# Optimization experiments

Measured on AMD Instinct MI355X. Metric: run time of the kernel, lower is better.

## Reference

```python
import jax, jax.numpy as jnp
import numpy as np

DIM = 512
HID = 2048
E = 16
B = 8
N = 2048
THRESHOLD = 0.8
CAP_FACTOR = 2.0  # eval mode
MIN_EXPERT_CAPACITY = 4
LOSS_COEF = 0.01
CAP = max(MIN_EXPERT_CAPACITY, min(N, int(N * CAP_FACTOR / E)))  # 256


def setup_inputs() -> dict:
    key = jax.random.key(0)
    k1, k2, k3, k4 = jax.random.split(key, 4)
    x = jax.random.normal(k1, (B, N, DIM), dtype=jnp.float32)
    w_gating = jax.random.normal(k2, (DIM, E), dtype=jnp.float32)
    std1 = 1.0 / np.sqrt(HID)
    std2 = 1.0 / np.sqrt(DIM)
    w1 = jax.random.uniform(k3, (E, DIM, HID), jnp.float32, -std1, std1)
    w2 = jax.random.uniform(k4, (E, HID, DIM), jnp.float32, -std2, std2)
    return {"x": x, "w_gating": w_gating, "w1": w1, "w2": w2}


def _gate(x, w_gating):
    # raw gate probabilities [B, N, E]
    raw = jax.nn.softmax(jnp.einsum('bnd,de->bne', x, w_gating), axis=-1)
    order = jnp.argsort(-raw, axis=-1)                      # descending sort indices
    sp = jnp.take_along_axis(raw, order, axis=-1)           # sorted probs (desc)
    cum = jnp.cumsum(sp, axis=-1)
    tm = cum >= THRESHOLD
    k = jnp.argmax(tm.astype(jnp.float32), axis=-1) + 1     # dynamic k per token
    k = jnp.where(jnp.any(tm, axis=-1), k, E)
    # select top-k in sorted order, renormalize
    rank = jnp.arange(E)
    sel = (rank < k[..., None]).astype(raw.dtype)           # [B,N,E] sorted order
    selp = sp * sel
    normp = selp / jnp.sum(selp, axis=-1, keepdims=True)
    # scatter back to expert order via inverse permutation
    inv = jnp.argsort(order, axis=-1)
    mask = jnp.take_along_axis(sel, inv, axis=-1)           # expert_masks [B,N,E]
    weights = jnp.take_along_axis(normp, inv, axis=-1)      # expert_weights
    # capacity: exclusive cumsum over tokens
    pos = (jnp.cumsum(mask, axis=-2) - mask) * mask
    mask = mask * (pos < float(CAP)).astype(mask.dtype)
    pos = pos * mask
    pos_tok = jnp.sum(pos, axis=-1).astype(jnp.int32)       # [B,N] (summed across experts, as in source)
    in_cap = (pos_tok < CAP).astype(raw.dtype)
    oh = jax.nn.one_hot(pos_tok, CAP, dtype=raw.dtype) * in_cap[..., None]  # [B,N,CAP]
    dispatch = mask[..., None] * oh[..., None, :]           # [B,N,E,CAP]
    combine = (weights * mask)[..., None] * oh[..., None, :]
    density = jnp.mean(mask, axis=-2)
    density_proxy = jnp.mean(raw, axis=-2)
    loss = jnp.mean(density_proxy * density) * float(E * E)
    loss = loss + 0.0 * jnp.mean(k.astype(jnp.float32))
    return dispatch, combine, loss


def reference(x, w_gating, w1, w2):
    dispatch, combine, loss = _gate(x, w_gating)
    expert_inputs = jnp.einsum('bnd,bnec->ebcd', x, dispatch)        # [E,B,CAP,D]
    ei = expert_inputs.reshape(E, B * CAP, DIM)
    hidden = jax.nn.gelu(jnp.einsum('end,edh->enh', ei, w1), approximate=False)
    eo = jnp.einsum('enh,ehd->end', hidden, w2).reshape(E, B, CAP, DIM)
    output = jnp.einsum('ebcd,bnec->bnd', eo, combine)               # [B,N,D]
    return output, loss * LOSS_COEF
```

## Files before the change

kernel.cpp:

```cpp
#include <hip/hip_runtime.h>
#include <math.h>

#define DIMC 512
#define HIDC 2048
#define EC   16
#define BC   8
#define NC   2048
#define CAPC 256
#define BN   (BC * NC)
#define THRESH 0.8f

typedef unsigned short u16;
typedef __attribute__((ext_vector_type(8))) __bf16 bf16x8;
typedef __attribute__((ext_vector_type(4))) float f32x4;

__device__ __forceinline__ float bf2f(unsigned u) {
    union { unsigned i; float f; } v; v.i = u << 16; return v.f;
}
__device__ __forceinline__ u16 f2bf(float f) {
    union { float f; unsigned i; } v; v.f = f;
    unsigned r = v.i + 0x7fff + ((v.i >> 16) & 1);
    return (u16)(r >> 16);
}
__device__ __forceinline__ float gelu_f(float x) {
    float u = 0.7978845608028654f * (x + 0.044715f * x * x * x);
    float t = __expf(2.f * u);
    float th = 1.f - 2.f / (t + 1.f);
    return 0.5f * x * (1.f + th);
}

__global__ void init_kernel(int* __restrict__ heads, int* __restrict__ pos_tok)
{
    int i = blockIdx.x * 256 + threadIdx.x;
    if (i < EC * BC * CAPC) heads[i] = -1;
    if (i < BN) pos_tok[i] = 0;
}

__global__ __launch_bounds__(256) void gate_kernel(const float* __restrict__ x,
                                                   const float* __restrict__ wg,
                                                   float* __restrict__ raw,
                                                   float* __restrict__ weights,
                                                   float* __restrict__ maskf)
{
    __shared__ float wlds[16][516];
    __shared__ float lg[16][16];
    int t = threadIdx.x;
    int tok16 = t >> 4, e = t & 15;
    int token = blockIdx.x * 16 + tok16;

    {
        const float4* wg4 = (const float4*)wg;
#pragma unroll
        for (int j = 0; j < 8; ++j) {
            int idx4 = j * 256 + t;
            float4 v = wg4[idx4];
            int d  = idx4 >> 2;
            int e0 = (idx4 & 3) * 4;
            wlds[e0 + 0][d] = v.x;
            wlds[e0 + 1][d] = v.y;
            wlds[e0 + 2][d] = v.z;
            wlds[e0 + 3][d] = v.w;
        }
    }
    __syncthreads();

    const float4* xr = (const float4*)(x + (size_t)token * DIMC);
    const float4* wl = (const float4*)&wlds[e][0];
    float a0 = 0.f, a1 = 0.f, a2 = 0.f, a3 = 0.f;
#pragma unroll 4
    for (int i = 0; i < 128; i += 4) {
        float4 xa = xr[i], xb = xr[i+1], xc = xr[i+2], xd = xr[i+3];
        float4 wa = wl[i], wb = wl[i+1], wc = wl[i+2], wd = wl[i+3];
        a0 = fmaf(xa.w, wa.w, fmaf(xa.z, wa.z, fmaf(xa.y, wa.y, fmaf(xa.x, wa.x, a0))));
        a1 = fmaf(xb.w, wb.w, fmaf(xb.z, wb.z, fmaf(xb.y, wb.y, fmaf(xb.x, wb.x, a1))));
        a2 = fmaf(xc.w, wc.w, fmaf(xc.z, wc.z, fmaf(xc.y, wc.y, fmaf(xc.x, wc.x, a2))));
        a3 = fmaf(xd.w, wd.w, fmaf(xd.z, wd.z, fmaf(xd.y, wd.y, fmaf(xd.x, wd.x, a3))));
    }
    float logit = (a0 + a1) + (a2 + a3);

    float m = logit;
#pragma unroll
    for (int off = 8; off >= 1; off >>= 1) m = fmaxf(m, __shfl_xor(m, off, 16));
    float p = expf(logit - m);
    float s = p;
#pragma unroll
    for (int off = 8; off >= 1; off >>= 1) s += __shfl_xor(s, off, 16);
    p = p / s;

    int rank = 0;
    float cum = p;
#pragma unroll
    for (int j = 1; j < 16; ++j) {
        float op = __shfl_xor(p, j, 16);
        int oidx = e ^ j;
        bool ahead = (op > p) || (op == p && oidx < e);
        if (ahead) { rank++; cum += op; }
    }
    bool tm = (cum >= THRESH);
    int kr = tm ? rank : (EC - 1);
#pragma unroll
    for (int off = 8; off >= 1; off >>= 1) kr = min(kr, __shfl_xor(kr, off, 16));
    bool sel = (rank <= kr);

    float dsel = sel ? p : 0.f;
    float denom = dsel;
#pragma unroll
    for (int off = 8; off >= 1; off >>= 1) denom += __shfl_xor(denom, off, 16);
    float w = sel ? (p / denom) : 0.f;

    size_t o = (size_t)token * EC + e;
    raw[o]     = p;
    weights[o] = w;
    maskf[o]   = sel ? 1.f : 0.f;
    (void)lg;
}

__global__ __launch_bounds__(64) void capacity_kernel(const float* __restrict__ raw,
                                                      float* __restrict__ maskf,
                                                      int* __restrict__ pos,
                                                      int* __restrict__ pos_tok,
                                                      float* __restrict__ density,
                                                      float* __restrict__ proxy)
{
    int t = blockIdx.x;
    int b = t / EC, e = t % EC;
    int lane = threadIdx.x;

    size_t idx = ((size_t)b * NC + lane) * EC + e;
    const size_t step = (size_t)64 * EC;
    float mv = maskf[idx];
    float rv = raw[idx];

    int count = 0;
    float rsum = 0.f;
    for (int n0 = 0; n0 < NC; n0 += 64) {
        float mn = 0.f, rn = 0.f;
        if (n0 + 64 < NC) { mn = maskf[idx + step]; rn = raw[idx + step]; }

        rsum += rv;
        unsigned long long bal = __ballot(mv != 0.f);
        int below = __popcll(bal & ((1ull << lane) - 1ull));
        int pval = 0;
        if (mv != 0.f) {
            pval = count + below;
            if (pval >= CAPC) { maskf[idx] = 0.f; pval = 0; }
            else if (pval > 0) atomicAdd(&pos_tok[b * NC + n0 + lane], pval);
        }
        pos[idx] = pval;
        count += __popcll(bal);

        idx += step; mv = mn; rv = rn;
    }
#pragma unroll
    for (int off = 32; off >= 1; off >>= 1) rsum += __shfl_xor(rsum, off);
    if (lane == 0) {
        int admitted = count < CAPC ? count : CAPC;
        density[t] = (float)admitted / (float)NC;
        proxy[t]   = rsum / (float)NC;
    }
}

__global__ __launch_bounds__(256) void build_kernel(const float* __restrict__ maskf,
                                                    const int* __restrict__ pos,
                                                    const int* __restrict__ pos_tok,
                                                    int* __restrict__ heads,
                                                    int* __restrict__ nxt,
                                                    int* __restrict__ node_tok)
{
    int id = blockIdx.x * 256 + threadIdx.x;
    int token = id >> 4, e = id & 15;
    if (maskf[id] == 0.f) return;
    int c = pos_tok[token];
    if (c >= CAPC) return;
    int b = token >> 11;
    int slot = (e * BC + b) * CAPC + c;
    int node = (e * BC + b) * CAPC + pos[id];
    node_tok[node] = token;
    nxt[node] = atomicExch(&heads[slot], node);
}

__global__ __launch_bounds__(256) void gather_ei_kernel(const float* __restrict__ x,
                                                        const int* __restrict__ heads,
                                                        const int* __restrict__ nxt,
                                                        const int* __restrict__ node_tok,
                                                        u16* __restrict__ ei)
{
    int slot = blockIdx.x * 4 + (threadIdx.x >> 6);
    int lane = threadIdx.x & 63;
    float a[8] = {0,0,0,0,0,0,0,0};
    int node = heads[slot];
    while (node >= 0) {
        const float4* xr = (const float4*)(x + (size_t)node_tok[node] * DIMC) + lane * 2;
        float4 v0 = xr[0], v1 = xr[1];
        a[0]+=v0.x; a[1]+=v0.y; a[2]+=v0.z; a[3]+=v0.w;
        a[4]+=v1.x; a[5]+=v1.y; a[6]+=v1.z; a[7]+=v1.w;
        node = nxt[node];
    }
    uint4 v;
    v.x = (unsigned)f2bf(a[0]) | ((unsigned)f2bf(a[1]) << 16);
    v.y = (unsigned)f2bf(a[2]) | ((unsigned)f2bf(a[3]) << 16);
    v.z = (unsigned)f2bf(a[4]) | ((unsigned)f2bf(a[5]) << 16);
    v.w = (unsigned)f2bf(a[6]) | ((unsigned)f2bf(a[7]) << 16);
    *(uint4*)(ei + (size_t)slot * DIMC + lane * 8) = v;
}

__global__ __launch_bounds__(256) void transpose_cvt_kernel(const float* __restrict__ in,
                                                            u16* __restrict__ out,
                                                            int R, int C)
{
    __shared__ float tile[64][65];
    size_t eoff = (size_t)blockIdx.z * R * C;
    int c0 = blockIdx.x * 64, r0 = blockIdx.y * 64;
    int tid = threadIdx.x;
    int rr = tid >> 4;
    int cc = (tid & 15) * 4;
#pragma unroll
    for (int i = 0; i < 4; ++i) {
        float4 v = *(const float4*)(in + eoff + (size_t)(r0 + rr + 16 * i) * C + c0 + cc);
        tile[rr + 16 * i][cc + 0] = v.x;
        tile[rr + 16 * i][cc + 1] = v.y;
        tile[rr + 16 * i][cc + 2] = v.z;
        tile[rr + 16 * i][cc + 3] = v.w;
    }
    __syncthreads();
    int c = tid >> 2;
    int r8 = (tid & 3) * 16;
    u16 buf[16];
#pragma unroll
    for (int j = 0; j < 16; ++j) buf[j] = f2bf(tile[r8 + j][c]);
    u16* op = out + eoff + (size_t)(c0 + c) * R + r0 + r8;
    *(uint4*)(op)     = *(uint4*)&buf[0];
    *(uint4*)(op + 8) = *(uint4*)&buf[8];
}

__device__ __forceinline__ void async_cp16(const u16* g, u16* l) {
    __builtin_amdgcn_global_load_lds(
        (const __attribute__((address_space(1))) unsigned*)g,
        (__attribute__((address_space(3))) unsigned*)l, 16, 0, 0);
}

template<int GELU>
__global__ __launch_bounds__(256) void gemm_bt_kernel(
    const u16* __restrict__ A, const u16* __restrict__ Bt, u16* __restrict__ C,
    int M, int N, int K, long sA, long sB, long sC)
{
    __shared__ __align__(16) u16 lds[2][2][128 * 64];
    int e = blockIdx.z;
    int bm = blockIdx.y * 128, bn = blockIdx.x * 128;
    int t = threadIdx.x, lane = t & 63, w = t >> 6;
    int wm = (w & 1) * 64, wn = (w >> 1) * 64;
    int q = lane >> 4, m16 = lane & 15;

    const u16* gA[4]; const u16* gB[4]; int lofs[4];
#pragma unroll
    for (int i = 0; i < 4; ++i) {
        int l = i * 256 + t, r = l >> 3, s = l & 7, c8 = s ^ (r & 7);
        gA[i] = A + (size_t)e * sA + (size_t)(bm + r) * K + c8 * 8;
        gB[i] = Bt + (size_t)e * sB + (size_t)(bn + r) * K + c8 * 8;
        lofs[i] = l * 8;
    }
    int aoff[4][2], boff[4][2];
#pragma unroll
    for (int i = 0; i < 4; ++i) {
        int ra = wm + i * 16 + m16, rb = wn + i * 16 + m16;
#pragma unroll
        for (int h = 0; h < 2; ++h) {
            int c8 = h * 4 + q;
            aoff[i][h] = (ra * 8 + (c8 ^ (ra & 7))) * 8;
            boff[i][h] = (rb * 8 + (c8 ^ (rb & 7))) * 8;
        }
    }

#pragma unroll
    for (int i = 0; i < 4; ++i) {
        async_cp16(gA[i], &lds[0][0][lofs[i]]);
        async_cp16(gB[i], &lds[0][1][lofs[i]]);
        gA[i] += 64; gB[i] += 64;
    }

    f32x4 acc[4][4] = {};
    int nk = K >> 6;
    for (int ki = 0; ki < nk; ++ki) {
        int cur = ki & 1, nx = cur ^ 1;
        __syncthreads();
        if (ki + 1 < nk) {
#pragma unroll
            for (int i = 0; i < 4; ++i) {
                async_cp16(gA[i], &lds[nx][0][lofs[i]]);
                async_cp16(gB[i], &lds[nx][1][lofs[i]]);
                gA[i] += 64; gB[i] += 64;
            }
        }
#pragma unroll
        for (int h = 0; h < 2; ++h) {
            bf16x8 af[4], bfr[4];
#pragma unroll
            for (int mt = 0; mt < 4; ++mt) af[mt] = *(const bf16x8*)&lds[cur][0][aoff[mt][h]];
#pragma unroll
            for (int nt = 0; nt < 4; ++nt) bfr[nt] = *(const bf16x8*)&lds[cur][1][boff[nt][h]];
#pragma unroll
            for (int mt = 0; mt < 4; ++mt)
#pragma unroll
                for (int nt = 0; nt < 4; ++nt)
                    acc[mt][nt] = __builtin_amdgcn_mfma_f32_16x16x32_bf16(
                        af[mt], bfr[nt], acc[mt][nt], 0, 0, 0);
        }
    }

    size_t cbase = (size_t)e * sC;
#pragma unroll
    for (int mt = 0; mt < 4; ++mt)
#pragma unroll
        for (int nt = 0; nt < 4; ++nt)
#pragma unroll
            for (int r2 = 0; r2 < 4; ++r2) {
                int row = bm + wm + mt * 16 + q * 4 + r2;
                int col = bn + wn + nt * 16 + m16;
                float v = acc[mt][nt][r2];
                if (GELU) v = gelu_f(v);
                C[cbase + (size_t)row * N + col] = f2bf(v);
            }
}

__global__ __launch_bounds__(256) void combine_kernel(const u16* __restrict__ eo,
                                                      const float* __restrict__ weights,
                                                      const float* __restrict__ maskf,
                                                      const int* __restrict__ pos_tok,
                                                      float* __restrict__ out)
{
    int token = blockIdx.x;
    int tid   = threadIdx.x;
    int b = token >> 11;
    int c = pos_tok[token];
    float a0 = 0.f, a1 = 0.f;
    if (c < CAPC) {
        const float* wr = weights + (size_t)token * EC;
        const float* mr = maskf   + (size_t)token * EC;
#pragma unroll
        for (int e = 0; e < EC; ++e) {
            float wm = wr[e] * mr[e];
            if (wm != 0.f) {
                const u16* src = eo + (((size_t)e * BC + b) * CAPC + c) * DIMC;
                unsigned u = *(const unsigned*)(src + 2 * tid);
                a0 += wm * bf2f(u & 0xffffu);
                a1 += wm * bf2f(u >> 16);
            }
        }
    }
    *(float2*)(out + (size_t)token * DIMC + 2 * tid) = make_float2(a0, a1);
}

__global__ void loss_kernel(const float* __restrict__ density,
                            const float* __restrict__ proxy,
                            float* __restrict__ out_loss)
{
    __shared__ float sh[BC * EC];
    int t = threadIdx.x;
    sh[t] = density[t] * proxy[t];
    __syncthreads();
    for (int s2 = (BC * EC) / 2; s2 >= 1; s2 >>= 1) {
        if (t < s2) sh[t] += sh[t + s2];
        __syncthreads();
    }
    if (t == 0)
        out_loss[0] = sh[0] * ((float)(EC * EC) / (float)(BC * EC)) * 0.01f;
}

extern "C" void kernel_launch(void* const* d_in, const int* in_sizes, int n_in,
                              void* d_out, int out_size, void* d_ws, size_t ws_size,
                              hipStream_t stream)
{
    const float* x  = (const float*)d_in[0];
    const float* wg = (const float*)d_in[1];
    const float* w1 = (const float*)d_in[2];
    const float* w2 = (const float*)d_in[3];
    float* out = (float*)d_out;

    char* ws = (char*)d_ws;
    size_t off = 0;
    auto alloc = [&](size_t bytes) -> void* {
        void* p = ws + off;
        off = (off + bytes + 255) & ~(size_t)255;
        return p;
    };
    float* raw      = (float*)alloc((size_t)BN * EC * 4);
    float* weights  = (float*)alloc((size_t)BN * EC * 4);
    float* maskf    = (float*)alloc((size_t)BN * EC * 4);
    int*   pos      = (int*)  alloc((size_t)BN * EC * 4);
    int*   pos_tok  = (int*)  alloc((size_t)BN * 4);
    int*   heads    = (int*)  alloc((size_t)EC * BC * CAPC * 4);
    int*   nxt      = (int*)  alloc((size_t)EC * BC * CAPC * 4);
    int*   node_tok = (int*)  alloc((size_t)EC * BC * CAPC * 4);
    float* density  = (float*)alloc(BC * EC * 4);
    float* proxy    = (float*)alloc(BC * EC * 4);
    u16*   ei_bf    = (u16*)alloc((size_t)EC * BC * CAPC * DIMC * 2);
    u16*   w1t      = (u16*)alloc((size_t)EC * DIMC * HIDC * 2);
    u16*   w2t      = (u16*)alloc((size_t)EC * HIDC * DIMC * 2);
    u16*   eo_bf    = (u16*)alloc((size_t)EC * BC * CAPC * DIMC * 2);
    size_t hid_full = (size_t)EC * BC * CAPC * HIDC * 2;
    int ngroups = (ws_size - off >= hid_full) ? 1 : 2;
    int EG = EC / ngroups;
    u16* hidden = (u16*)alloc((size_t)EG * BC * CAPC * HIDC * 2);

    (void)in_sizes; (void)n_in; (void)out_size;

    init_kernel<<<(EC * BC * CAPC + 255) / 256, 256, 0, stream>>>(heads, pos_tok);
    transpose_cvt_kernel<<<dim3(HIDC / 64, DIMC / 64, EC), 256, 0, stream>>>(w1, w1t, DIMC, HIDC);
    transpose_cvt_kernel<<<dim3(DIMC / 64, HIDC / 64, EC), 256, 0, stream>>>(w2, w2t, HIDC, DIMC);

    gate_kernel<<<BN / 16, 256, 0, stream>>>(x, wg, raw, weights, maskf);
    capacity_kernel<<<BC * EC, 64, 0, stream>>>(raw, maskf, pos, pos_tok, density, proxy);
    build_kernel<<<BN * EC / 256, 256, 0, stream>>>(maskf, pos, pos_tok, heads, nxt, node_tok);
    gather_ei_kernel<<<EC * BC * CAPC / 4, 256, 0, stream>>>(x, heads, nxt, node_tok, ei_bf);

    for (int g = 0; g < ngroups; ++g) {
        const u16* Ag  = ei_bf + (size_t)g * EG * BC * CAPC * DIMC;
        const u16* B1g = w1t   + (size_t)g * EG * DIMC * HIDC;
        gemm_bt_kernel<1><<<dim3(HIDC / 128, (BC * CAPC) / 128, EG), 256, 0, stream>>>(
            Ag, B1g, hidden, BC * CAPC, HIDC, DIMC,
            (long)BC * CAPC * DIMC, (long)HIDC * DIMC, (long)BC * CAPC * HIDC);
        const u16* B2g = w2t + (size_t)g * EG * HIDC * DIMC;
        u16* Eg = eo_bf + (size_t)g * EG * BC * CAPC * DIMC;
        gemm_bt_kernel<0><<<dim3(DIMC / 128, (BC * CAPC) / 128, EG), 256, 0, stream>>>(
            hidden, B2g, Eg, BC * CAPC, DIMC, HIDC,
            (long)BC * CAPC * HIDC, (long)DIMC * HIDC, (long)BC * CAPC * DIMC);
    }

    combine_kernel<<<BN, 256, 0, stream>>>(eo_bf, weights, maskf, pos_tok, out);
    loss_kernel<<<1, BC * EC, 0, stream>>>(density, proxy, out + (size_t)BN * DIMC);
}
```

Baseline: 470.6 us.

## Replace 128x128 expert GEMM with 256x256 tile, 8-wave ping-pong pipelined kernel

New measurement: 492.6 us. 4.7% more time.

```diff
diff --git a/kernel.cpp b/kernel.cpp
--- a/kernel.cpp
+++ b/kernel.cpp
@@ -239,83 +239,166 @@
         (__attribute__((address_space(3))) unsigned*)l, 16, 0, 0);
 }
 
+#define GFENCE() asm volatile("" ::: "memory")
+#define BAR() do { GFENCE(); __builtin_amdgcn_s_barrier(); GFENCE(); } while (0)
+
 template<int GELU>
-__global__ __launch_bounds__(256) void gemm_bt_kernel(
+__global__ __launch_bounds__(512, 2) void gemm256_kernel(
     const u16* __restrict__ A, const u16* __restrict__ Bt, u16* __restrict__ C,
     int M, int N, int K, long sA, long sB, long sC)
 {
-    __shared__ __align__(16) u16 lds[2][2][128 * 64];
-    int e = blockIdx.z;
-    int bm = blockIdx.y * 128, bn = blockIdx.x * 128;
-    int t = threadIdx.x, lane = t & 63, w = t >> 6;
-    int wm = (w & 1) * 64, wn = (w >> 1) * 64;
-    int q = lane >> 4, m16 = lane & 15;
-
-    const u16* gA[4]; const u16* gB[4]; int lofs[4];
-#pragma unroll
-    for (int i = 0; i < 4; ++i) {
-        int l = i * 256 + t, r = l >> 3, s = l & 7, c8 = s ^ (r & 7);
-        gA[i] = A + (size_t)e * sA + (size_t)(bm + r) * K + c8 * 8;
-        gB[i] = Bt + (size_t)e * sB + (size_t)(bn + r) * K + c8 * 8;
-        lofs[i] = l * 8;
-    }
-    int aoff[4][2], boff[4][2];
-#pragma unroll
-    for (int i = 0; i < 4; ++i) {
-        int ra = wm + i * 16 + m16, rb = wn + i * 16 + m16;
-#pragma unroll
-        for (int h = 0; h < 2; ++h) {
-            int c8 = h * 4 + q;
-            aoff[i][h] = (ra * 8 + (c8 ^ (ra & 7))) * 8;
-            boff[i][h] = (rb * 8 + (c8 ^ (rb & 7))) * 8;
+    __shared__ __align__(16) u16 lds[2][2][2][8192];
+    const int e = blockIdx.z;
+    const int bm = blockIdx.y * 256, bn = blockIdx.x * 256;
+    const int t = threadIdx.x, lane = t & 63, w = t >> 6;
+    const int wm = w & 1;
+    const int wn = w >> 1;
+    const int bh = wn >> 1;
+    const int q = lane >> 4, m16 = lane & 15;
+
+    const u16* g[2][2][2];
+    int lofs[2];
+#pragma unroll
+    for (int j = 0; j < 2; ++j) {
+        int l = j * 512 + t, r = l >> 3, c = (l & 7) ^ (r & 7);
+        lofs[j] = l * 8;
+        g[0][0][j] = A  + (size_t)e * sA + (size_t)(bm + r) * K + c * 8;
+        g[0][1][j] = A  + (size_t)e * sA + (size_t)(bm + 128 + r) * K + c * 8;
+        g[1][0][j] = Bt + (size_t)e * sB + (size_t)(bn + r) * K + c * 8;
+        g[1][1][j] = Bt + (size_t)e * sB + (size_t)(bn + 128 + r) * K + c * 8;
+    }
+
+    int aro[8], bro[4];
+#pragma unroll
+    for (int mt = 0; mt < 8; ++mt) {
+        int r = mt * 16 + m16;
+        aro[mt] = r * 64 + (q ^ (r & 7)) * 8;
+    }
+#pragma unroll
+    for (int nt = 0; nt < 4; ++nt) {
+        int r = (wn & 1) * 64 + nt * 16 + m16;
+        bro[nt] = r * 64 + (q ^ (r & 7)) * 8;
+    }
+
+    auto STAGE = [&](int buf, int op, int half) {
+#pragma unroll
+        for (int j = 0; j < 2; ++j) {
+            async_cp16(g[op][half][j], &lds[buf][op][half][lofs[j]]);
+            g[op][half][j] += 64;
         }
-    }
-
-#pragma unroll
-    for (int i = 0; i < 4; ++i) {
-        async_cp16(gA[i], &lds[0][0][lofs[i]]);
-        async_cp16(gB[i], &lds[0][1][lofs[i]]);
-        gA[i] += 64; gB[i] += 64;
-    }
-
-    f32x4 acc[4][4] = {};
-    int nk = K >> 6;
-    for (int ki = 0; ki < nk; ++ki) {
-        int cur = ki & 1, nx = cur ^ 1;
-        __syncthreads();
-        if (ki + 1 < nk) {
-#pragma unroll
-            for (int i = 0; i < 4; ++i) {
-                async_cp16(gA[i], &lds[nx][0][lofs[i]]);
-                async_cp16(gB[i], &lds[nx][1][lofs[i]]);
-                gA[i] += 64; gB[i] += 64;
-            }
+    };
+
+    const int nk = K >> 6;
+    STAGE(0, 1, 0); STAGE(0, 1, 1);
+    STAGE(0, 0, 0); STAGE(0, 0, 1);
+    if (nk > 1) {
+        STAGE(1, 1, 0); STAGE(1, 1, 1);
+        asm volatile("s_waitcnt vmcnt(4)" ::: "memory");
+    } else {
+        asm volatile("s_waitcnt vmcnt(0)" ::: "memory");
+    }
+    BAR();
+
+    f32x4 acc[8][4] = {};
+    for (int ti = 0; ti < nk; ++ti) {
+        const int cur = ti & 1, nx = cur ^ 1;
+        const u16* lA = &lds[cur][0][wm][0];
+        const u16* lB = &lds[cur][1][bh][0];
+        bf16x8 a0[4][2], a1[4][2], b01[2][2], b23[2][2];
+
+#pragma unroll
+        for (int mt = 0; mt < 4; ++mt)
+#pragma unroll
+            for (int kk = 0; kk < 2; ++kk)
+                a0[mt][kk] = *(const bf16x8*)&lA[aro[mt] ^ (kk * 32)];
+#pragma unroll
+        for (int nt = 0; nt < 2; ++nt)
+#pragma unroll
+            for (int kk = 0; kk < 2; ++kk)
+                b01[nt][kk] = *(const bf16x8*)&lB[bro[nt] ^ (kk * 32)];
+        if (ti + 1 < nk) STAGE(nx, 0, 0);
+        BAR();
+        asm volatile("s_waitcnt lgkmcnt(0)" ::: "memory");
+        __builtin_amdgcn_s_setprio(1);
+#pragma unroll
+        for (int mt = 0; mt < 4; ++mt)
+#pragma unroll
+            for (int nt = 0; nt < 2; ++nt)
+#pragma unroll
+                for (int kk = 0; kk < 2; ++kk)
+                    acc[mt][nt] = __builtin_amdgcn_mfma_f32_16x16x32_bf16(
+                        a0[mt][kk], b01[nt][kk], acc[mt][nt], 0, 0, 0);
+        __builtin_amdgcn_s_setprio(0);
+        BAR();
+
+#pragma unroll
+        for (int nt = 0; nt < 2; ++nt)
+#pragma unroll
+            for (int kk = 0; kk < 2; ++kk)
+                b23[nt][kk] = *(const bf16x8*)&lB[bro[2 + nt] ^ (kk * 32)];
+        if (ti + 1 < nk) STAGE(nx, 0, 1);
+        BAR();
+        asm volatile("s_waitcnt lgkmcnt(0)" ::: "memory");
+        __builtin_amdgcn_s_setprio(1);
+#pragma unroll
+        for (int mt = 0; mt < 4; ++mt)
+#pragma unroll
+            for (int nt = 0; nt < 2; ++nt)
+#pragma unroll
+                for (int kk = 0; kk < 2; ++kk)
+                    acc[mt][2 + nt] = __builtin_amdgcn_mfma_f32_16x16x32_bf16(
+                        a0[mt][kk], b23[nt][kk], acc[mt][2 + nt], 0, 0, 0);
+        __builtin_amdgcn_s_setprio(0);
+        BAR();
+
+#pragma unroll
+        for (int mt = 0; mt < 4; ++mt)
+#pragma unroll
+            for (int kk = 0; kk < 2; ++kk)
+                a1[mt][kk] = *(const bf16x8*)&lA[aro[4 + mt] ^ (kk * 32)];
+        if (ti + 2 < nk) STAGE(cur, 1, 0);
+        BAR();
+        asm volatile("s_waitcnt lgkmcnt(0)" ::: "memory");
+        __builtin_amdgcn_s_setprio(1);
+#pragma unroll
+        for (int mt = 0; mt < 4; ++mt)
+#pragma unroll
+            for (int nt = 0; nt < 2; ++nt)
+#pragma unroll
+                for (int kk = 0; kk < 2; ++kk)
+                    acc[4 + mt][2 + nt] = __builtin_amdgcn_mfma_f32_16x16x32_bf16(
+                        a1[mt][kk], b23[nt][kk], acc[4 + mt][2 + nt], 0, 0, 0);
+        __builtin_amdgcn_s_setprio(0);
+        BAR();
+
+        if (ti + 2 < nk) STAGE(cur, 1, 1);
+        BAR();
+        __builtin_amdgcn_s_setprio(1);
+#pragma unroll
+        for (int mt = 0; mt < 4; ++mt)
+#pragma unroll
+            for (int nt = 0; nt < 2; ++nt)
+#pragma unroll
+                for (int kk = 0; kk < 2; ++kk)
+                    acc[4 + mt][nt] = __builtin_amdgcn_mfma_f32_16x16x32_bf16(
+                        a1[mt][kk], b01[nt][kk], acc[4 + mt][nt], 0, 0, 0);
+        __builtin_amdgcn_s_setprio(0);
+        if (ti + 1 < nk) {
+            if (ti + 2 < nk) asm volatile("s_waitcnt vmcnt(4)" ::: "memory");
+            else             asm volatile("s_waitcnt vmcnt(0)" ::: "memory");
         }
-#pragma unroll
-        for (int h = 0; h < 2; ++h) {
-            bf16x8 af[4], bfr[4];
-#pragma unroll
-            for (int mt = 0; mt < 4; ++mt) af[mt] = *(const bf16x8*)&lds[cur][0][aoff[mt][h]];
-#pragma unroll
-            for (int nt = 0; nt < 4; ++nt) bfr[nt] = *(const bf16x8*)&lds[cur][1][boff[nt][h]];
-#pragma unroll
-            for (int mt = 0; mt < 4; ++mt)
-#pragma unroll
-                for (int nt = 0; nt < 4; ++nt)
-                    acc[mt][nt] = __builtin_amdgcn_mfma_f32_16x16x32_bf16(
-                        af[mt], bfr[nt], acc[mt][nt], 0, 0, 0);
-        }
-    }
-
-    size_t cbase = (size_t)e * sC;
-#pragma unroll
-    for (int mt = 0; mt < 4; ++mt)
+        BAR();
+    }
+
+    const size_t cbase = (size_t)e * sC;
+#pragma unroll
+    for (int mt = 0; mt < 8; ++mt)
 #pragma unroll
         for (int nt = 0; nt < 4; ++nt)
 #pragma unroll
             for (int r2 = 0; r2 < 4; ++r2) {
-                int row = bm + wm + mt * 16 + q * 4 + r2;
-                int col = bn + wn + nt * 16 + m16;
+                int row = bm + wm * 128 + mt * 16 + q * 4 + r2;
+                int col = bn + wn * 64 + nt * 16 + m16;
                 float v = acc[mt][nt][r2];
                 if (GELU) v = gelu_f(v);
                 C[cbase + (size_t)row * N + col] = f2bf(v);
@@ -416,12 +499,12 @@
     for (int g = 0; g < ngroups; ++g) {
         const u16* Ag  = ei_bf + (size_t)g * EG * BC * CAPC * DIMC;
         const u16* B1g = w1t   + (size_t)g * EG * DIMC * HIDC;
-        gemm_bt_kernel<1><<<dim3(HIDC / 128, (BC * CAPC) / 128, EG), 256, 0, stream>>>(
+        gemm256_kernel<1><<<dim3(HIDC / 256, (BC * CAPC) / 256, EG), 512, 0, stream>>>(
             Ag, B1g, hidden, BC * CAPC, HIDC, DIMC,
             (long)BC * CAPC * DIMC, (long)HIDC * DIMC, (long)BC * CAPC * HIDC);
         const u16* B2g = w2t + (size_t)g * EG * HIDC * DIMC;
         u16* Eg = eo_bf + (size_t)g * EG * BC * CAPC * DIMC;
-        gemm_bt_kernel<0><<<dim3(DIMC / 128, (BC * CAPC) / 128, EG), 256, 0, stream>>>(
+        gemm256_kernel<0><<<dim3(DIMC / 256, (BC * CAPC) / 256, EG), 512, 0, stream>>>(
             hidden, B2g, Eg, BC * CAPC, DIMC, HIDC,
             (long)BC * CAPC * HIDC, (long)DIMC * HIDC, (long)BC * CAPC * DIMC);
     }
```
